# Performance work log

Measured on AMD Instinct MI355X. Metric: run time of the kernel, lower is better.

Reference implementation:

```python
import jax, jax.numpy as jnp
import numpy as np

HIDDEN = 1280
HEADS = 16
HEAD_DIM = HIDDEN // HEADS  # 80
INTER = 4608
DEPTH = 4
WIN = 64                     # tokens per attention window
FULL_BLOCKS = (3,)           # fullatt_block_indexes
EPS = 1e-6
SEQ = 3072


def setup_inputs() -> dict:
    key = jax.random.key(0)
    ks = jax.random.split(key, 20)
    sc = lambda *s: 0.02
    inp = {
        "x": jax.random.normal(ks[0], (SEQ, HIDDEN), jnp.float32),
        "rotary_pos_emb": jax.random.uniform(ks[1], (SEQ, HEAD_DIM // 2), jnp.float32) * 3.0,
        "s_aux": jax.random.normal(ks[2], (HEADS,), jnp.float32),
        "ln1_w": jnp.ones((DEPTH, HIDDEN), jnp.float32),
        "ln1_b": jnp.zeros((DEPTH, HIDDEN), jnp.float32),
        "qkv_w": jax.random.normal(ks[3], (DEPTH, HIDDEN, 3 * HIDDEN), jnp.float32) * 0.02,
        "qkv_b": jnp.zeros((DEPTH, 3 * HIDDEN), jnp.float32),
        "proj_w": jax.random.normal(ks[4], (DEPTH, HIDDEN, HIDDEN), jnp.float32) * 0.02,
        "proj_b": jnp.zeros((DEPTH, HIDDEN), jnp.float32),
        "ln2_w": jnp.ones((DEPTH, HIDDEN), jnp.float32),
        "ln2_b": jnp.zeros((DEPTH, HIDDEN), jnp.float32),
        "gate_w": jax.random.normal(ks[5], (DEPTH, HIDDEN, INTER), jnp.float32) * 0.02,
        "gate_b": jnp.zeros((DEPTH, INTER), jnp.float32),
        "up_w": jax.random.normal(ks[6], (DEPTH, HIDDEN, INTER), jnp.float32) * 0.02,
        "up_b": jnp.zeros((DEPTH, INTER), jnp.float32),
        "down_w": jax.random.normal(ks[7], (DEPTH, INTER, HIDDEN), jnp.float32) * 0.02,
        "down_b": jnp.zeros((DEPTH, HIDDEN), jnp.float32),
    }
    return inp


def _layer_norm(x, w, b):
    mu = jnp.mean(x, axis=-1, keepdims=True)
    var = jnp.mean(jnp.square(x - mu), axis=-1, keepdims=True)
    return (x - mu) * jax.lax.rsqrt(var + EPS) * w + b


def _rotate_half(x):
    x1, x2 = jnp.split(x, 2, axis=-1)
    return jnp.concatenate([-x2, x1], axis=-1)


def _apply_rotary(q, k, rot):
    # q,k: [S, H, D]; rot: [S, D/2]
    emb = jnp.concatenate([rot, rot], axis=-1)          # [S, D]
    cos = jnp.cos(emb)[:, None, :]
    sin = jnp.sin(emb)[:, None, :]
    q = q * cos + _rotate_half(q) * sin
    k = k * cos + _rotate_half(k) * sin
    return q, k


def _attention_with_sinks(q, k, v, s_aux):
    # q,k,v: [B, T, H, D]; block-diagonal within each of B windows.
    scale = 1.0 / jnp.sqrt(jnp.asarray(HEAD_DIM, q.dtype))
    scores = jnp.einsum("bqhd,bkhd->bhqk", q, k) * scale      # [B,H,q,k]
    sink = s_aux[None, :, None]                                # [1,H,1]
    m = jnp.maximum(jnp.max(scores, axis=-1), sink)            # [B,H,q]
    p = jnp.exp(scores - m[..., None])                         # [B,H,q,k]
    denom = jnp.sum(p, axis=-1) + jnp.exp(sink - m)            # [B,H,q]
    out = jnp.einsum("bhqk,bkhd->bqhd", p, v)
    out = out / jnp.transpose(denom, (0, 2, 1))[..., None]     # [B,q,H,D]
    return out


def reference(x, rotary_pos_emb, s_aux, ln1_w, ln1_b, qkv_w, qkv_b, proj_w, proj_b,
              ln2_w, ln2_b, gate_w, gate_b, up_w, up_b, down_w, down_b):
    S = x.shape[0]
    h = x
    for l in range(DEPTH):
        # --- attention ---
        hn = _layer_norm(h, ln1_w[l], ln1_b[l])
        qkv = hn @ qkv_w[l] + qkv_b[l]                          # [S, 3*HIDDEN]
        qkv = qkv.reshape(S, 3, HEADS, HEAD_DIM)
        q, k, v = qkv[:, 0], qkv[:, 1], qkv[:, 2]               # [S,H,D]
        q, k = _apply_rotary(q, k, rotary_pos_emb)
        if l in FULL_BLOCKS:
            B, T = 1, S                                         # full attention
        else:
            B, T = S // WIN, WIN                                # windowed (varlen block-diag)
        qw = q.reshape(B, T, HEADS, HEAD_DIM)
        kw = k.reshape(B, T, HEADS, HEAD_DIM)
        vw = v.reshape(B, T, HEADS, HEAD_DIM)
        o = _attention_with_sinks(qw, kw, vw, s_aux)            # [B,T,H,D]
        o = o.reshape(S, HIDDEN) @ proj_w[l] + proj_b[l]
        h = h + o
        # --- gated SiLU MLP ---
        hn = _layer_norm(h, ln2_w[l], ln2_b[l])
        g = jax.nn.silu(hn @ gate_w[l] + gate_b[l]) * (hn @ up_w[l] + up_b[l])
        h = h + g @ down_w[l] + down_b[l]
    return h
```

## Files before the change

kernel.cpp:

```cpp
#include <hip/hip_runtime.h>
#include <math.h>

typedef unsigned short u16;
typedef unsigned int u32;

using bf16x8 = __attribute__((ext_vector_type(8))) __bf16;
using f32x4  = __attribute__((ext_vector_type(4))) float;

#define SEQ 3072
#define HID 1280
#define NHEADS 16
#define HDIM 80
#define INTER 4608

#define LOG2E 1.44269504088896f
#define M2C   11.5415603f

__device__ __forceinline__ u16 f2bf(float f) {
    __bf16 h = (__bf16)f;
    return __builtin_bit_cast(u16, h);
}

__device__ __forceinline__ void gld16(const void* g, void* l) {
    __builtin_amdgcn_global_load_lds((const __attribute__((address_space(1))) void*)g,
                                     (__attribute__((address_space(3))) void*)l,
                                     16, 0, 0);
}

__device__ __forceinline__ bf16x8 frag8(const u16* base, int row, int ks, int quad) {
    int c = ks * 4 + quad;
    return *(const bf16x8*)&base[(row * 8 + (c ^ (row & 7))) * 8];
}

__global__ __launch_bounds__(256) void transpose_pack(const float* __restrict__ src,
                                                      u16* __restrict__ dst, int K, int N) {
    __shared__ float tile[32][33];
    int l = blockIdx.z;
    const float* s = src + (size_t)l * K * N;
    u16* d = dst + (size_t)l * N * K;
    int n0 = blockIdx.x * 32, k0 = blockIdx.y * 32;
    int tx = threadIdx.x & 31, ty = threadIdx.x >> 5;
#pragma unroll
    for (int i = 0; i < 4; i++) {
        int k = ty + i * 8;
        tile[k][tx] = s[(size_t)(k0 + k) * N + n0 + tx];
    }
    __syncthreads();
#pragma unroll
    for (int i = 0; i < 4; i++) {
        int n = ty + i * 8;
        d[(size_t)(n0 + n) * K + k0 + tx] = f2bf(tile[tx][n]);
    }
}

__global__ __launch_bounds__(256) void transpose_pack_gu(const float* __restrict__ src,
                                                         u16* __restrict__ dst, int K, int N,
                                                         int which) {
    __shared__ float tile[32][33];
    int l = blockIdx.z;
    const float* s = src + (size_t)l * K * N;
    u16* d = dst + (size_t)l * (2 * N) * K;
    int n0 = blockIdx.x * 32, k0 = blockIdx.y * 32;
    int tx = threadIdx.x & 31, ty = threadIdx.x >> 5;
#pragma unroll
    for (int i = 0; i < 4; i++) {
        int k = ty + i * 8;
        tile[k][tx] = s[(size_t)(k0 + k) * N + n0 + tx];
    }
    __syncthreads();
#pragma unroll
    for (int i = 0; i < 4; i++) {
        int n = ty + i * 8;
        int g = n0 + n;
        int n2 = ((g >> 4) << 5) | (g & 15) | (which << 4);
        d[(size_t)n2 * K + k0 + tx] = f2bf(tile[tx][n]);
    }
}

__global__ __launch_bounds__(256) void ln_kernel(const float* __restrict__ x,
                                                 const float* __restrict__ w,
                                                 const float* __restrict__ b,
                                                 u16* __restrict__ out) {
    int row = blockIdx.x;
    const float* xr = x + (size_t)row * HID;
    float v[5]; float s = 0.f, s2 = 0.f;
#pragma unroll
    for (int i = 0; i < 5; i++) { float t = xr[threadIdx.x + i * 256]; v[i] = t; s += t; s2 += t * t; }
#pragma unroll
    for (int off = 32; off > 0; off >>= 1) { s += __shfl_down(s, off); s2 += __shfl_down(s2, off); }
    __shared__ float red[8];
    int wv = threadIdx.x >> 6;
    if ((threadIdx.x & 63) == 0) { red[wv] = s; red[wv + 4] = s2; }
    __syncthreads();
    s  = red[0] + red[1] + red[2] + red[3];
    s2 = red[4] + red[5] + red[6] + red[7];
    float mu  = s * (1.f / HID);
    float var = s2 * (1.f / HID) - mu * mu;
    float rstd = rsqrtf(var + 1e-6f);
#pragma unroll
    for (int i = 0; i < 5; i++) {
        int col = threadIdx.x + i * 256;
        out[(size_t)row * HID + col] = f2bf((v[i] - mu) * rstd * w[col] + b[col]);
    }
}

__global__ __launch_bounds__(256) void qkv_pack(const float* __restrict__ qkv,
                                                const float* __restrict__ rot,
                                                u16* __restrict__ Qp, u16* __restrict__ Kp,
                                                u16* __restrict__ Vt) {
    const float QSC = 0.111803398874989485f * LOG2E;
    int s0 = blockIdx.x * 64, h = blockIdx.y;
    int tid = threadIdx.x;
    __shared__ u16 vlds[80 * 66];
    for (int idx = tid; idx < 64 * 40; idx += 256) {
        int r = idx / 40, d = idx - r * 40;
        const float* base = qkv + (size_t)(s0 + r) * 3840 + h * 80;
        float sn, cs;
        __sincosf(rot[(size_t)(s0 + r) * 40 + d], &sn, &cs);
        float q1 = base[d], q2 = base[d + 40];
        float k1 = base[1280 + d], k2 = base[1280 + d + 40];
        size_t ro = ((size_t)h * SEQ + s0 + r) * 128;
        Qp[ro + d]      = f2bf((q1 * cs - q2 * sn) * QSC);
        Qp[ro + d + 40] = f2bf((q2 * cs + q1 * sn) * QSC);
        Kp[ro + d]      = f2bf(k1 * cs - k2 * sn);
        Kp[ro + d + 40] = f2bf(k2 * cs + k1 * sn);
    }
    for (int idx = tid; idx < 64 * 48; idx += 256) {
        int r = idx / 48, d = 80 + (idx - r * 48);
        size_t ro = ((size_t)h * SEQ + s0 + r) * 128;
        Qp[ro + d] = 0; Kp[ro + d] = 0;
    }
    for (int idx = tid; idx < 64 * 80; idx += 256) {
        int r = idx / 80, d = idx - r * 80;
        vlds[d * 66 + r] = f2bf(qkv[(size_t)(s0 + r) * 3840 + 2560 + h * 80 + d]);
    }
    __syncthreads();
    for (int idx = tid; idx < 80 * 64; idx += 256) {
        int d = idx >> 6, ky = idx & 63;
        Vt[((size_t)h * 80 + d) * SEQ + s0 + ky] = vlds[d * 66 + ky];
    }
}

template<int EPI>
__global__ __launch_bounds__(512, 2) void gemm256(const u16* __restrict__ A,
                                                  const u16* __restrict__ B,
                                                  const float* __restrict__ bias0,
                                                  const float* __restrict__ bias1,
                                                  float* __restrict__ outf,
                                                  u16* __restrict__ outh,
                                                  int N, int K) {
    __shared__ u16 sbuf[73728];
    int tid = threadIdx.x, lane = tid & 63, wave = tid >> 6;
    int quad = lane >> 4, r15 = lane & 15;
    int wm = wave >> 2, wn = wave & 3;

    int nwg = gridDim.x;
    int q8 = nwg >> 3, r8 = nwg & 7;
    int xcd = blockIdx.x & 7, j = blockIdx.x >> 3;
    int wg = (xcd < r8 ? xcd * (q8 + 1) : r8 * (q8 + 1) + (xcd - r8) * q8) + j;
    int bx = wg >> 4, by = wg & 15;
    int mBase = by * 192, nBase = bx * 256;

    int rs = tid >> 3, cs = tid & 7;
    int c0 = cs ^ (rs & 7);
    const u16* gA = A + (size_t)(mBase + rs) * K + c0 * 8;
    const u16* gB = B + (size_t)(nBase + rs) * K + c0 * 8;
    int nK = K >> 6;

    f32x4 acc[6][4] = {};

    auto stageA = [&](int kt, int jl) {
        gld16(gA + (size_t)kt * 64 + (size_t)(jl * 64) * K,
              &sbuf[(kt & 1) * 12288 + jl * 4096 + wave * 512]);
    };
    auto stageB = [&](int kt, int jl) {
        gld16(gB + (size_t)kt * 64 + (size_t)(jl * 64) * K,
              &sbuf[24576 + (kt % 3) * 16384 + jl * 4096 + wave * 512]);
    };

#pragma unroll
    for (int jl = 0; jl < 3; jl++) stageA(0, jl);
#pragma unroll
    for (int jl = 0; jl < 4; jl++) stageB(0, jl);
#pragma unroll
    for (int jl = 0; jl < 4; jl++) stageB(1, jl);
    asm volatile("s_waitcnt vmcnt(4)" ::: "memory");
    __builtin_amdgcn_s_barrier();

    for (int kt = 0; kt < nK; kt++) {
        const u16* Ab = &sbuf[(kt & 1) * 12288];
        const u16* Bb = &sbuf[24576 + (kt % 3) * 16384];
        bool preA = (kt + 1 < nK), preB = (kt + 2 < nK);
#pragma unroll
        for (int ks = 0; ks < 2; ks++) {
            bf16x8 af[6], bf[4];
#pragma unroll
            for (int mi = 0; mi < 6; mi++)
                af[mi] = frag8(Ab, wm * 96 + mi * 16 + r15, ks, quad);
#pragma unroll
            for (int ni = 0; ni < 4; ni++)
                bf[ni] = frag8(Bb, wn * 64 + ni * 16 + r15, ks, quad);
            if (ks == 0) {
                if (preA) { stageA(kt + 1, 0); stageA(kt + 1, 1); stageA(kt + 1, 2); }
            } else {
                if (preB) { stageB(kt + 2, 0); stageB(kt + 2, 1); stageB(kt + 2, 2); stageB(kt + 2, 3); }
            }
            __builtin_amdgcn_s_barrier();
            __builtin_amdgcn_s_setprio(1);
#pragma unroll
            for (int mi = 0; mi < 6; mi++)
#pragma unroll
                for (int ni = 0; ni < 4; ni++)
                    acc[mi][ni] = __builtin_amdgcn_mfma_f32_16x16x32_bf16(
                        af[mi], bf[ni], acc[mi][ni], 0, 0, 0);
            __builtin_amdgcn_s_setprio(0);
            if (ks == 0) __builtin_amdgcn_s_barrier();
        }
        if (preB)      { asm volatile("s_waitcnt vmcnt(4)" ::: "memory"); }
        else if (preA) { asm volatile("s_waitcnt vmcnt(0)" ::: "memory"); }
        __builtin_amdgcn_s_barrier();
    }

    if constexpr (EPI == 0) {
#pragma unroll
        for (int ni = 0; ni < 4; ni++) {
            int col = nBase + wn * 64 + ni * 16 + r15;
            float bv = bias0[col];
#pragma unroll
            for (int a = 0; a < 6; a++)
#pragma unroll
                for (int jj = 0; jj < 4; jj++) {
                    int row = mBase + wm * 96 + a * 16 + quad * 4 + jj;
                    outf[(size_t)row * N + col] = acc[a][ni][jj] + bv;
                }
        }
    } else {
#pragma unroll
        for (int pp = 0; pp < 2; pp++) {
            int col = (nBase >> 1) + wn * 32 + pp * 16 + r15;
            float gb = bias0[col], ub = bias1[col];
#pragma unroll
            for (int a = 0; a < 6; a++)
#pragma unroll
                for (int jj = 0; jj < 4; jj++) {
                    int row = mBase + wm * 96 + a * 16 + quad * 4 + jj;
                    float g = acc[a][2 * pp][jj] + gb;
                    float u = acc[a][2 * pp + 1][jj] + ub;
                    float sg = g / (1.f + __expf(-g));
                    outh[(size_t)row * INTER + col] = f2bf(sg * u);
                }
        }
    }
}

template<int BM, int EPI>
__global__ __launch_bounds__(512, 2) void gemm8(const u16* __restrict__ A,
                                                const u16* __restrict__ B,
                                                const float* __restrict__ bias0,
                                                const float* __restrict__ bias1,
                                                const float* __restrict__ res,
                                                float* __restrict__ outf,
                                                u16* __restrict__ outh,
                                                int N, int K) {
    constexpr int MT   = 3072 / BM;
    constexpr int MF   = BM / 32;
    constexpr int LA   = BM / 64;
    constexpr int LT   = LA + 2;
    constexpr int ABUF = BM * 64;
    constexpr int BUFU = ABUF + 8192;
    __shared__ u16 sbuf[3 * BUFU];

    int tid = threadIdx.x, lane = tid & 63, wave = tid >> 6;
    int quad = lane >> 4, r15 = lane & 15;
    int wm = wave >> 2, wn = wave & 3;

    int nwg = gridDim.x;
    int q8 = nwg >> 3, r8 = nwg & 7;
    int xcd = blockIdx.x & 7, j = blockIdx.x >> 3;
    int wg = (xcd < r8 ? xcd * (q8 + 1) : r8 * (q8 + 1) + (xcd - r8) * q8) + j;
    int bx = wg / MT, by = wg % MT;
    int mBase = by * BM, nBase = bx * 128;

    int rs = tid >> 3, cs = tid & 7;
    int c0 = cs ^ (rs & 7);
    const u16* gA = A + (size_t)(mBase + rs) * K + c0 * 8;
    const u16* gB = B + (size_t)(nBase + rs) * K + c0 * 8;
    int nK = K >> 6;

    f32x4 acc[MF][2] = {};

    auto stage1 = [&](int kt, int jl) {
        int b = kt % 3;
        if (jl < LA) {
            gld16(gA + (size_t)kt * 64 + (size_t)(jl * 64) * K,
                  &sbuf[b * BUFU + jl * 4096 + wave * 512]);
        } else {
            int i = jl - LA;
            gld16(gB + (size_t)kt * 64 + (size_t)(i * 64) * K,
                  &sbuf[b * BUFU + ABUF + i * 4096 + wave * 512]);
        }
    };

#pragma unroll
    for (int jl = 0; jl < LT; jl++) stage1(0, jl);
#pragma unroll
    for (int jl = 0; jl < LT; jl++) stage1(1, jl);
    asm volatile("s_waitcnt vmcnt(4)" ::: "memory");
    __builtin_amdgcn_s_barrier();

    for (int kt = 0; kt < nK; kt++) {
        const u16* Ab = &sbuf[(kt % 3) * BUFU];
        const u16* Bb = Ab + ABUF;
        bool pre = (kt + 2 < nK);
#pragma unroll
        for (int ks = 0; ks < 2; ks++) {
            bf16x8 af[MF], bf[2];
#pragma unroll
            for (int mi = 0; mi < MF; mi++)
                af[mi] = frag8(Ab, wm * (BM / 2) + mi * 16 + r15, ks, quad);
#pragma unroll
            for (int ni = 0; ni < 2; ni++)
                bf[ni] = frag8(Bb, wn * 32 + ni * 16 + r15, ks, quad);
            if (pre) {
#pragma unroll
                for (int jl = 0; jl < LT / 2; jl++) stage1(kt + 2, ks * (LT / 2) + jl);
            }
            __builtin_amdgcn_s_barrier();
            __builtin_amdgcn_s_setprio(1);
#pragma unroll
            for (int mi = 0; mi < MF; mi++)
#pragma unroll
                for (int ni = 0; ni < 2; ni++)
                    acc[mi][ni] = __builtin_amdgcn_mfma_f32_16x16x32_bf16(
                        af[mi], bf[ni], acc[mi][ni], 0, 0, 0);
            __builtin_amdgcn_s_setprio(0);
            if (ks == 0) __builtin_amdgcn_s_barrier();
        }
        if (pre) {
            asm volatile("s_waitcnt vmcnt(4)" ::: "memory");
        } else if (kt + 1 < nK) {
            asm volatile("s_waitcnt vmcnt(0)" ::: "memory");
        }
        __builtin_amdgcn_s_barrier();
    }

#pragma unroll
    for (int ni = 0; ni < 2; ni++) {
        int col = nBase + wn * 32 + ni * 16 + r15;
        float bv = bias0[col];
#pragma unroll
        for (int mi = 0; mi < MF; mi++)
#pragma unroll
            for (int jj = 0; jj < 4; jj++) {
                int row = mBase + wm * (BM / 2) + mi * 16 + quad * 4 + jj;
                float v = acc[mi][ni][jj] + bv;
                if constexpr (EPI == 1) v += res[(size_t)row * N + col];
                outf[(size_t)row * N + col] = v;
            }
    }
}

template<int QR>
__global__ __launch_bounds__(256) void attn_kernel(const u16* __restrict__ Qp,
                                                   const u16* __restrict__ Kp,
                                                   const u16* __restrict__ Vt,
                                                   const float* __restrict__ s_aux,
                                                   u16* __restrict__ out) {
    constexpr int MH = QR / 64;
    __shared__ u16 q_lds[QR * 128];
    __shared__ u16 k_lds[8192];
    __shared__ u16 v_lds[5120];
    __shared__ u16 p_lds[QR * 72];

    int qt = blockIdx.x, h = blockIdx.y;
    int tid = threadIdx.x, lane = tid & 63, wave = tid >> 6;
    int quad = lane >> 4, r15 = lane & 15;

    const u16* Qh = Qp + (size_t)h * SEQ * 128;
    const u16* Kh = Kp + (size_t)h * SEQ * 128;
    const u16* Vh = Vt + (size_t)h * 80 * SEQ;

    {
        int q0 = qt * QR;
#pragma unroll
        for (int i = 0; i < QR / 16; i++) {
            int slot = i * 256 + tid;
            int row = slot >> 4, cc = slot & 15;
            int c = cc ^ (row & 7);
            gld16(Qh + (size_t)(q0 + row) * 128 + c * 8, &q_lds[(i * 256 + wave * 64) * 8]);
        }
    }
    __syncthreads();
    bf16x8 aq[MH][3];
#pragma unroll
    for (int mh = 0; mh < MH; mh++)
#pragma unroll
        for (int ks = 0; ks < 3; ks++) {
            int row = wave * (16 * MH) + mh * 16 + r15;
            int c = ks * 4 + quad;
            aq[mh][ks] = *(const bf16x8*)&q_lds[(row * 16 + (c ^ (row & 7))) * 8];
        }

    float l_j[MH][4] = {};
    f32x4 ov[MH][5] = {};

    int nT = (QR == 64) ? 1 : (SEQ / 64);
    int tBase = (QR == 64) ? qt : 0;
    for (int t = 0; t < nT; t++) {
        int key0 = (tBase + t) * 64;
        __syncthreads();
#pragma unroll
        for (int i = 0; i < 4; i++) {
            int slot = i * 256 + wave * 64 + lane;
            int row = slot >> 4, cc = slot & 15;
            int c = cc ^ (row & 7);
            gld16(Kh + (size_t)(key0 + row) * 128 + c * 8, &k_lds[(i * 256 + wave * 64) * 8]);
        }
#pragma unroll
        for (int i = 0; i < 2; i++) {
            int slot = i * 256 + wave * 64 + lane;
            int row = slot >> 3, cc = slot & 7;
            int c = cc ^ (row & 7);
            gld16(Vh + (size_t)row * SEQ + key0 + c * 8, &v_lds[(i * 256 + wave * 64) * 8]);
        }
        if (wave < 2) {
            int slot = 512 + wave * 64 + lane;
            int row = slot >> 3, cc = slot & 7;
            int c = cc ^ (row & 7);
            gld16(Vh + (size_t)row * SEQ + key0 + c * 8, &v_lds[(512 + wave * 64) * 8]);
        }
        __syncthreads();

        f32x4 sc[MH][4] = {};
#pragma unroll
        for (int nt = 0; nt < 4; nt++)
#pragma unroll
            for (int ks = 0; ks < 3; ks++) {
                int row = nt * 16 + r15;
                int c = ks * 4 + quad;
                bf16x8 bk = *(const bf16x8*)&k_lds[(row * 16 + (c ^ (row & 7))) * 8];
#pragma unroll
                for (int mh = 0; mh < MH; mh++)
                    sc[mh][nt] = __builtin_amdgcn_mfma_f32_16x16x32_bf16(aq[mh][ks], bk, sc[mh][nt], 0, 0, 0);
            }
#pragma unroll
        for (int mh = 0; mh < MH; mh++)
#pragma unroll
            for (int nt = 0; nt < 4; nt++)
#pragma unroll
                for (int jj = 0; jj < 4; jj++) {
                    float p = __builtin_amdgcn_exp2f(sc[mh][nt][jj] - M2C);
                    l_j[mh][jj] += p;
                    p_lds[(wave * 16 * MH + mh * 16 + quad * 4 + jj) * 72 + nt * 16 + r15] = f2bf(p);
                }
        asm volatile("s_waitcnt lgkmcnt(0)" ::: "memory");
        bf16x8 ap[MH][2];
#pragma unroll
        for (int mh = 0; mh < MH; mh++)
#pragma unroll
            for (int ks = 0; ks < 2; ks++)
                ap[mh][ks] = *(const bf16x8*)&p_lds[(wave * 16 * MH + mh * 16 + r15) * 72 + ks * 32 + quad * 8];
#pragma unroll
        for (int t5 = 0; t5 < 5; t5++)
#pragma unroll
            for (int ks = 0; ks < 2; ks++) {
                int d = t5 * 16 + r15;
                int c = ks * 4 + quad;
                bf16x8 bv = *(const bf16x8*)&v_lds[(d * 8 + (c ^ (d & 7))) * 8];
#pragma unroll
                for (int mh = 0; mh < MH; mh++)
                    ov[mh][t5] = __builtin_amdgcn_mfma_f32_16x16x32_bf16(ap[mh][ks], bv, ov[mh][t5], 0, 0, 0);
            }
    }
#pragma unroll
    for (int mh = 0; mh < MH; mh++)
#pragma unroll
        for (int off = 1; off < 16; off <<= 1)
#pragma unroll
            for (int jj = 0; jj < 4; jj++)
                l_j[mh][jj] += __shfl_xor(l_j[mh][jj], off, 64);
    float sink = s_aux[h];
    float se = __builtin_amdgcn_exp2f(sink * LOG2E - M2C);
#pragma unroll
    for (int mh = 0; mh < MH; mh++)
#pragma unroll
        for (int jj = 0; jj < 4; jj++) l_j[mh][jj] = 1.f / (l_j[mh][jj] + se);
#pragma unroll
    for (int mh = 0; mh < MH; mh++)
#pragma unroll
        for (int t5 = 0; t5 < 5; t5++)
#pragma unroll
            for (int jj = 0; jj < 4; jj++) {
                int row = qt * QR + wave * 16 * MH + mh * 16 + quad * 4 + jj;
                int d = t5 * 16 + r15;
                out[(size_t)row * HID + h * 80 + d] = f2bf(ov[mh][t5][jj] * l_j[mh][jj]);
            }
}

__global__ __launch_bounds__(256) void copy4_kernel(const float4* __restrict__ src,
                                                    float4* __restrict__ dst) {
    size_t i = (size_t)blockIdx.x * 256 + threadIdx.x;
    dst[i] = src[i];
}

extern "C" void kernel_launch(void* const* d_in, const int* in_sizes, int n_in,
                              void* d_out, int out_size, void* d_ws, size_t ws_size,
                              hipStream_t stream) {
    const float* x      = (const float*)d_in[0];
    const float* rot    = (const float*)d_in[1];
    const float* s_aux  = (const float*)d_in[2];
    const float* ln1_w  = (const float*)d_in[3];
    const float* ln1_b  = (const float*)d_in[4];
    const float* qkv_w  = (const float*)d_in[5];
    const float* qkv_b  = (const float*)d_in[6];
    const float* proj_w = (const float*)d_in[7];
    const float* proj_b = (const float*)d_in[8];
    const float* ln2_w  = (const float*)d_in[9];
    const float* ln2_b  = (const float*)d_in[10];
    const float* gate_w = (const float*)d_in[11];
    const float* gate_b = (const float*)d_in[12];
    const float* up_w   = (const float*)d_in[13];
    const float* up_b   = (const float*)d_in[14];
    const float* down_w = (const float*)d_in[15];
    const float* down_b = (const float*)d_in[16];

    char* ws = (char*)d_ws;
    size_t off = 0;
    auto alloc = [&](size_t n) -> char* {
        char* p = ws + off; off += (n + 255) & ~(size_t)255; return p;
    };
    u16* wt_qkv  = (u16*)alloc((size_t)4 * 3840 * 1280 * 2);
    u16* wt_proj = (u16*)alloc((size_t)4 * 1280 * 1280 * 2);
    u16* wt_gu   = (u16*)alloc((size_t)4 * 9216 * 1280 * 2);
    u16* wt_down = (u16*)alloc((size_t)4 * 1280 * 4608 * 2);
    float* h     = (float*)alloc((size_t)3072 * 1280 * 4);
    u16*  xn     = (u16*)alloc((size_t)3072 * 1280 * 2);
    float* gbuf  = (float*)alloc((size_t)3072 * 4608 * 4);
    float* qkvb  = gbuf;
    u16*  attnb  = (u16*)alloc((size_t)3072 * 1280 * 2);
    float* ubuf  = (float*)alloc((size_t)3072 * 4608 * 4);
    u16*  mbuf   = (u16*)alloc((size_t)3072 * 4608 * 2);
    u16* Qp  = (u16*)ubuf;
    u16* Kp  = Qp + (size_t)NHEADS * SEQ * 128;
    u16* Vtp = Kp + (size_t)NHEADS * SEQ * 128;

    transpose_pack<<<dim3(120, 40, 4), 256, 0, stream>>>(qkv_w,  wt_qkv,  1280, 3840);
    transpose_pack<<<dim3(40,  40, 4), 256, 0, stream>>>(proj_w, wt_proj, 1280, 1280);
    transpose_pack_gu<<<dim3(144, 40, 4), 256, 0, stream>>>(gate_w, wt_gu, 1280, 4608, 0);
    transpose_pack_gu<<<dim3(144, 40, 4), 256, 0, stream>>>(up_w,   wt_gu, 1280, 4608, 1);
    transpose_pack<<<dim3(40, 144, 4), 256, 0, stream>>>(down_w, wt_down, 4608, 1280);

    copy4_kernel<<<3840, 256, 0, stream>>>((const float4*)x, (float4*)h);

    for (int l = 0; l < 4; l++) {
        ln_kernel<<<3072, 256, 0, stream>>>(h, ln1_w + l * 1280, ln1_b + l * 1280, xn);
        gemm256<0><<<240, 512, 0, stream>>>(xn, wt_qkv + (size_t)l * 3840 * 1280,
                                            qkv_b + l * 3840, nullptr,
                                            qkvb, nullptr, 3840, 1280);
        qkv_pack<<<dim3(48, 16), 256, 0, stream>>>(qkvb, rot, Qp, Kp, Vtp);
        if (l == 3)
            attn_kernel<128><<<dim3(SEQ / 128, 16), 256, 0, stream>>>(Qp, Kp, Vtp, s_aux, attnb);
        else
            attn_kernel<64><<<dim3(SEQ / 64, 16), 256, 0, stream>>>(Qp, Kp, Vtp, s_aux, attnb);
        gemm8<128, 1><<<240, 512, 0, stream>>>(attnb, wt_proj + (size_t)l * 1280 * 1280,
                                               proj_b + l * 1280, nullptr, h,
                                               h, nullptr, 1280, 1280);
        ln_kernel<<<3072, 256, 0, stream>>>(h, ln2_w + l * 1280, ln2_b + l * 1280, xn);
        gemm256<2><<<576, 512, 0, stream>>>(xn, wt_gu + (size_t)l * 9216 * 1280,
                                            gate_b + l * 4608, up_b + l * 4608,
                                            nullptr, mbuf, 9216, 1280);
        float* outp = (l == 3) ? (float*)d_out : h;
        gemm8<128, 1><<<240, 512, 0, stream>>>(mbuf, wt_down + (size_t)l * 4608 * 1280,
                                               down_b + l * 1280, nullptr, h,
                                               outp, nullptr, 1280, 4608);
    }
}
```

Before: 1.467 ms.

## Restructure GEMM pipelines with split A/B buffering and prefetch attention K/V tiles

The 256-wide GEMM drops the mid-iteration barriers, precomputes swizzled LDS offsets, and splits its k-step loop into two explicit halves. The proj/down GEMM is specialised to 128x128 tiles with double-buffered A and triple-buffered B, a smaller shared allocation, and launch bounds raised to 4 blocks per CU. The attention kernel now prefetches the next K/V tile into registers while computing on the current one, then writes it to LDS between barriers. Together these aim to hide memory latency and cut barrier stalls, at the cost of more register pressure and a risk of LDS races once the intermediate barriers are gone.

Measured after the change: 1.522 ms. +3.8%, slower.

```diff
diff --git a/kernel.cpp b/kernel.cpp
--- a/kernel.cpp
+++ b/kernel.cpp
@@ -167,6 +167,21 @@
     const u16* gB = B + (size_t)(nBase + rs) * K + c0 * 8;
     int nK = K >> 6;
 
+    int offA[2][6], offB[2][4];
+#pragma unroll
+    for (int ks = 0; ks < 2; ks++) {
+#pragma unroll
+        for (int mi = 0; mi < 6; mi++) {
+            int row = wm * 96 + mi * 16 + r15, c = ks * 4 + quad;
+            offA[ks][mi] = (row * 8 + (c ^ (row & 7))) * 8;
+        }
+#pragma unroll
+        for (int ni = 0; ni < 4; ni++) {
+            int row = wn * 64 + ni * 16 + r15, c = ks * 4 + quad;
+            offB[ks][ni] = (row * 8 + (c ^ (row & 7))) * 8;
+        }
+    }
+
     f32x4 acc[6][4] = {};
 
     auto stageA = [&](int kt, int jl) {
@@ -182,6 +197,7 @@
     for (int jl = 0; jl < 3; jl++) stageA(0, jl);
 #pragma unroll
     for (int jl = 0; jl < 4; jl++) stageB(0, jl);
+    asm volatile("" ::: "memory");
 #pragma unroll
     for (int jl = 0; jl < 4; jl++) stageB(1, jl);
     asm volatile("s_waitcnt vmcnt(4)" ::: "memory");
@@ -191,21 +207,14 @@
         const u16* Ab = &sbuf[(kt & 1) * 12288];
         const u16* Bb = &sbuf[24576 + (kt % 3) * 16384];
         bool preA = (kt + 1 < nK), preB = (kt + 2 < nK);
-#pragma unroll
-        for (int ks = 0; ks < 2; ks++) {
+        {
             bf16x8 af[6], bf[4];
 #pragma unroll
-            for (int mi = 0; mi < 6; mi++)
-                af[mi] = frag8(Ab, wm * 96 + mi * 16 + r15, ks, quad);
-#pragma unroll
-            for (int ni = 0; ni < 4; ni++)
-                bf[ni] = frag8(Bb, wn * 64 + ni * 16 + r15, ks, quad);
-            if (ks == 0) {
-                if (preA) { stageA(kt + 1, 0); stageA(kt + 1, 1); stageA(kt + 1, 2); }
-            } else {
-                if (preB) { stageB(kt + 2, 0); stageB(kt + 2, 1); stageB(kt + 2, 2); stageB(kt + 2, 3); }
-            }
-            __builtin_amdgcn_s_barrier();
+            for (int mi = 0; mi < 6; mi++) af[mi] = *(const bf16x8*)&Ab[offA[0][mi]];
+#pragma unroll
+            for (int ni = 0; ni < 4; ni++) bf[ni] = *(const bf16x8*)&Bb[offB[0][ni]];
+            if (preA) { stageA(kt + 1, 0); stageA(kt + 1, 1); stageA(kt + 1, 2); }
+            asm volatile("" ::: "memory");
             __builtin_amdgcn_s_setprio(1);
 #pragma unroll
             for (int mi = 0; mi < 6; mi++)
@@ -214,7 +223,22 @@
                     acc[mi][ni] = __builtin_amdgcn_mfma_f32_16x16x32_bf16(
                         af[mi], bf[ni], acc[mi][ni], 0, 0, 0);
             __builtin_amdgcn_s_setprio(0);
-            if (ks == 0) __builtin_amdgcn_s_barrier();
+        }
+        {
+            bf16x8 af[6], bf[4];
+#pragma unroll
+            for (int mi = 0; mi < 6; mi++) af[mi] = *(const bf16x8*)&Ab[offA[1][mi]];
+#pragma unroll
+            for (int ni = 0; ni < 4; ni++) bf[ni] = *(const bf16x8*)&Bb[offB[1][ni]];
+            if (preB) { stageB(kt + 2, 0); stageB(kt + 2, 1); stageB(kt + 2, 2); stageB(kt + 2, 3); }
+            __builtin_amdgcn_s_setprio(1);
+#pragma unroll
+            for (int mi = 0; mi < 6; mi++)
+#pragma unroll
+                for (int ni = 0; ni < 4; ni++)
+                    acc[mi][ni] = __builtin_amdgcn_mfma_f32_16x16x32_bf16(
+                        af[mi], bf[ni], acc[mi][ni], 0, 0, 0);
+            __builtin_amdgcn_s_setprio(0);
         }
         if (preB)      { asm volatile("s_waitcnt vmcnt(4)" ::: "memory"); }
         else if (preA) { asm volatile("s_waitcnt vmcnt(0)" ::: "memory"); }
@@ -253,23 +277,14 @@
     }
 }
 
-template<int BM, int EPI>
-__global__ __launch_bounds__(512, 2) void gemm8(const u16* __restrict__ A,
+template<int EPI>
+__global__ __launch_bounds__(512, 4) void gemm8(const u16* __restrict__ A,
                                                 const u16* __restrict__ B,
                                                 const float* __restrict__ bias0,
-                                                const float* __restrict__ bias1,
                                                 const float* __restrict__ res,
                                                 float* __restrict__ outf,
-                                                u16* __restrict__ outh,
                                                 int N, int K) {
-    constexpr int MT   = 3072 / BM;
-    constexpr int MF   = BM / 32;
-    constexpr int LA   = BM / 64;
-    constexpr int LT   = LA + 2;
-    constexpr int ABUF = BM * 64;
-    constexpr int BUFU = ABUF + 8192;
-    __shared__ u16 sbuf[3 * BUFU];
-
+    __shared__ u16 sbuf[40960];
     int tid = threadIdx.x, lane = tid & 63, wave = tid >> 6;
     int quad = lane >> 4, r15 = lane & 15;
     int wm = wave >> 2, wn = wave & 3;
@@ -278,8 +293,8 @@
     int q8 = nwg >> 3, r8 = nwg & 7;
     int xcd = blockIdx.x & 7, j = blockIdx.x >> 3;
     int wg = (xcd < r8 ? xcd * (q8 + 1) : r8 * (q8 + 1) + (xcd - r8) * q8) + j;
-    int bx = wg / MT, by = wg % MT;
-    int mBase = by * BM, nBase = bx * 128;
+    int bx = wg / 24, by = wg % 24;
+    int mBase = by * 128, nBase = bx * 128;
 
     int rs = tid >> 3, cs = tid & 7;
     int c0 = cs ^ (rs & 7);
@@ -287,60 +302,81 @@
     const u16* gB = B + (size_t)(nBase + rs) * K + c0 * 8;
     int nK = K >> 6;
 
-    f32x4 acc[MF][2] = {};
-
-    auto stage1 = [&](int kt, int jl) {
-        int b = kt % 3;
-        if (jl < LA) {
-            gld16(gA + (size_t)kt * 64 + (size_t)(jl * 64) * K,
-                  &sbuf[b * BUFU + jl * 4096 + wave * 512]);
-        } else {
-            int i = jl - LA;
-            gld16(gB + (size_t)kt * 64 + (size_t)(i * 64) * K,
-                  &sbuf[b * BUFU + ABUF + i * 4096 + wave * 512]);
-        }
+    int offA[2][4], offB[2][2];
+#pragma unroll
+    for (int ks = 0; ks < 2; ks++) {
+#pragma unroll
+        for (int mi = 0; mi < 4; mi++) {
+            int row = wm * 64 + mi * 16 + r15, c = ks * 4 + quad;
+            offA[ks][mi] = (row * 8 + (c ^ (row & 7))) * 8;
+        }
+#pragma unroll
+        for (int ni = 0; ni < 2; ni++) {
+            int row = wn * 32 + ni * 16 + r15, c = ks * 4 + quad;
+            offB[ks][ni] = (row * 8 + (c ^ (row & 7))) * 8;
+        }
+    }
+
+    f32x4 acc[4][2] = {};
+
+    auto stageA = [&](int kt, int jl) {
+        gld16(gA + (size_t)kt * 64 + (size_t)(jl * 64) * K,
+              &sbuf[(kt & 1) * 8192 + jl * 4096 + wave * 512]);
     };
-
-#pragma unroll
-    for (int jl = 0; jl < LT; jl++) stage1(0, jl);
-#pragma unroll
-    for (int jl = 0; jl < LT; jl++) stage1(1, jl);
-    asm volatile("s_waitcnt vmcnt(4)" ::: "memory");
+    auto stageB = [&](int kt, int jl) {
+        gld16(gB + (size_t)kt * 64 + (size_t)(jl * 64) * K,
+              &sbuf[16384 + (kt % 3) * 8192 + jl * 4096 + wave * 512]);
+    };
+
+#pragma unroll
+    for (int jl = 0; jl < 2; jl++) stageA(0, jl);
+#pragma unroll
+    for (int jl = 0; jl < 2; jl++) stageB(0, jl);
+    asm volatile("" ::: "memory");
+#pragma unroll
+    for (int jl = 0; jl < 2; jl++) stageB(1, jl);
+    asm volatile("s_waitcnt vmcnt(2)" ::: "memory");
     __builtin_amdgcn_s_barrier();
 
     for (int kt = 0; kt < nK; kt++) {
-        const u16* Ab = &sbuf[(kt % 3) * BUFU];
-        const u16* Bb = Ab + ABUF;
-        bool pre = (kt + 2 < nK);
-#pragma unroll
-        for (int ks = 0; ks < 2; ks++) {
-            bf16x8 af[MF], bf[2];
-#pragma unroll
-            for (int mi = 0; mi < MF; mi++)
-                af[mi] = frag8(Ab, wm * (BM / 2) + mi * 16 + r15, ks, quad);
-#pragma unroll
-            for (int ni = 0; ni < 2; ni++)
-                bf[ni] = frag8(Bb, wn * 32 + ni * 16 + r15, ks, quad);
-            if (pre) {
-#pragma unroll
-                for (int jl = 0; jl < LT / 2; jl++) stage1(kt + 2, ks * (LT / 2) + jl);
-            }
-            __builtin_amdgcn_s_barrier();
+        const u16* Ab = &sbuf[(kt & 1) * 8192];
+        const u16* Bb = &sbuf[16384 + (kt % 3) * 8192];
+        bool preA = (kt + 1 < nK), preB = (kt + 2 < nK);
+        {
+            bf16x8 af[4], bf[2];
+#pragma unroll
+            for (int mi = 0; mi < 4; mi++) af[mi] = *(const bf16x8*)&Ab[offA[0][mi]];
+#pragma unroll
+            for (int ni = 0; ni < 2; ni++) bf[ni] = *(const bf16x8*)&Bb[offB[0][ni]];
+            if (preA) { stageA(kt + 1, 0); stageA(kt + 1, 1); }
+            asm volatile("" ::: "memory");
             __builtin_amdgcn_s_setprio(1);
 #pragma unroll
-            for (int mi = 0; mi < MF; mi++)
+            for (int mi = 0; mi < 4; mi++)
 #pragma unroll
                 for (int ni = 0; ni < 2; ni++)
                     acc[mi][ni] = __builtin_amdgcn_mfma_f32_16x16x32_bf16(
                         af[mi], bf[ni], acc[mi][ni], 0, 0, 0);
             __builtin_amdgcn_s_setprio(0);
-            if (ks == 0) __builtin_amdgcn_s_barrier();
-        }
-        if (pre) {
-            asm volatile("s_waitcnt vmcnt(4)" ::: "memory");
-        } else if (kt + 1 < nK) {
-            asm volatile("s_waitcnt vmcnt(0)" ::: "memory");
-        }
+        }
+        {
+            bf16x8 af[4], bf[2];
+#pragma unroll
+            for (int mi = 0; mi < 4; mi++) af[mi] = *(const bf16x8*)&Ab[offA[1][mi]];
+#pragma unroll
+            for (int ni = 0; ni < 2; ni++) bf[ni] = *(const bf16x8*)&Bb[offB[1][ni]];
+            if (preB) { stageB(kt + 2, 0); stageB(kt + 2, 1); }
+            __builtin_amdgcn_s_setprio(1);
+#pragma unroll
+            for (int mi = 0; mi < 4; mi++)
+#pragma unroll
+                for (int ni = 0; ni < 2; ni++)
+                    acc[mi][ni] = __builtin_amdgcn_mfma_f32_16x16x32_bf16(
+                        af[mi], bf[ni], acc[mi][ni], 0, 0, 0);
+            __builtin_amdgcn_s_setprio(0);
+        }
+        if (preB)      { asm volatile("s_waitcnt vmcnt(2)" ::: "memory"); }
+        else if (preA) { asm volatile("s_waitcnt vmcnt(0)" ::: "memory"); }
         __builtin_amdgcn_s_barrier();
     }
 
@@ -349,10 +385,10 @@
         int col = nBase + wn * 32 + ni * 16 + r15;
         float bv = bias0[col];
 #pragma unroll
-        for (int mi = 0; mi < MF; mi++)
+        for (int mi = 0; mi < 4; mi++)
 #pragma unroll
             for (int jj = 0; jj < 4; jj++) {
-                int row = mBase + wm * (BM / 2) + mi * 16 + quad * 4 + jj;
+                int row = mBase + wm * 64 + mi * 16 + quad * 4 + jj;
                 float v = acc[mi][ni][jj] + bv;
                 if constexpr (EPI == 1) v += res[(size_t)row * N + col];
                 outf[(size_t)row * N + col] = v;
@@ -406,30 +442,52 @@
 
     int nT = (QR == 64) ? 1 : (SEQ / 64);
     int tBase = (QR == 64) ? qt : 0;
+
+    {
+        int key0 = tBase * 64;
+#pragma unroll
+        for (int i = 0; i < 4; i++) {
+            int slot = i * 256 + tid;
+            int row = slot >> 4, c = (slot & 15) ^ (row & 7);
+            gld16(Kh + (size_t)(key0 + row) * 128 + c * 8, &k_lds[(i * 256 + wave * 64) * 8]);
+        }
+#pragma unroll
+        for (int i = 0; i < 2; i++) {
+            int slot = i * 256 + tid;
+            int row = slot >> 3, c = (slot & 7) ^ (row & 7);
+            gld16(Vh + (size_t)row * SEQ + key0 + c * 8, &v_lds[(i * 256 + wave * 64) * 8]);
+        }
+        if (tid < 128) {
+            int slot = 512 + tid;
+            int row = slot >> 3, c = (slot & 7) ^ (row & 7);
+            gld16(Vh + (size_t)row * SEQ + key0 + c * 8, &v_lds[(512 + (tid >> 6) * 64) * 8]);
+        }
+    }
+    __syncthreads();
+
     for (int t = 0; t < nT; t++) {
-        int key0 = (tBase + t) * 64;
-        __syncthreads();
-#pragma unroll
-        for (int i = 0; i < 4; i++) {
-            int slot = i * 256 + wave * 64 + lane;
-            int row = slot >> 4, cc = slot & 15;
-            int c = cc ^ (row & 7);
-            gld16(Kh + (size_t)(key0 + row) * 128 + c * 8, &k_lds[(i * 256 + wave * 64) * 8]);
-        }
-#pragma unroll
-        for (int i = 0; i < 2; i++) {
-            int slot = i * 256 + wave * 64 + lane;
-            int row = slot >> 3, cc = slot & 7;
-            int c = cc ^ (row & 7);
-            gld16(Vh + (size_t)row * SEQ + key0 + c * 8, &v_lds[(i * 256 + wave * 64) * 8]);
-        }
-        if (wave < 2) {
-            int slot = 512 + wave * 64 + lane;
-            int row = slot >> 3, cc = slot & 7;
-            int c = cc ^ (row & 7);
-            gld16(Vh + (size_t)row * SEQ + key0 + c * 8, &v_lds[(512 + wave * 64) * 8]);
-        }
-        __syncthreads();
+        bool pf = (t + 1 < nT);
+        uint4 kreg[4], vreg[3];
+        if (pf) {
+            int keyN = (tBase + t + 1) * 64;
+#pragma unroll
+            for (int i = 0; i < 4; i++) {
+                int slot = i * 256 + tid;
+                int row = slot >> 4, c = (slot & 15) ^ (row & 7);
+                kreg[i] = *(const uint4*)(Kh + (size_t)(keyN + row) * 128 + c * 8);
+            }
+#pragma unroll
+            for (int i = 0; i < 2; i++) {
+                int slot = i * 256 + tid;
+                int row = slot >> 3, c = (slot & 7) ^ (row & 7);
+                vreg[i] = *(const uint4*)(Vh + (size_t)row * SEQ + keyN + c * 8);
+            }
+            if (tid < 128) {
+                int slot = 512 + tid;
+                int row = slot >> 3, c = (slot & 7) ^ (row & 7);
+                vreg[2] = *(const uint4*)(Vh + (size_t)row * SEQ + keyN + c * 8);
+            }
+        }
 
         f32x4 sc[MH][4] = {};
 #pragma unroll
@@ -471,6 +529,16 @@
                 for (int mh = 0; mh < MH; mh++)
                     ov[mh][t5] = __builtin_amdgcn_mfma_f32_16x16x32_bf16(ap[mh][ks], bv, ov[mh][t5], 0, 0, 0);
             }
+
+        if (pf) {
+            __syncthreads();
+#pragma unroll
+            for (int i = 0; i < 4; i++) ((uint4*)k_lds)[i * 256 + tid] = kreg[i];
+#pragma unroll
+            for (int i = 0; i < 2; i++) ((uint4*)v_lds)[i * 256 + tid] = vreg[i];
+            if (tid < 128) ((uint4*)v_lds)[512 + tid] = vreg[2];
+            __syncthreads();
+        }
     }
 #pragma unroll
     for (int mh = 0; mh < MH; mh++)
@@ -562,16 +630,14 @@
             attn_kernel<128><<<dim3(SEQ / 128, 16), 256, 0, stream>>>(Qp, Kp, Vtp, s_aux, attnb);
         else
             attn_kernel<64><<<dim3(SEQ / 64, 16), 256, 0, stream>>>(Qp, Kp, Vtp, s_aux, attnb);
-        gemm8<128, 1><<<240, 512, 0, stream>>>(attnb, wt_proj + (size_t)l * 1280 * 1280,
-                                               proj_b + l * 1280, nullptr, h,
-                                               h, nullptr, 1280, 1280);
+        gemm8<1><<<240, 512, 0, stream>>>(attnb, wt_proj + (size_t)l * 1280 * 1280,
+                                          proj_b + l * 1280, h, h, 1280, 1280);
         ln_kernel<<<3072, 256, 0, stream>>>(h, ln2_w + l * 1280, ln2_b + l * 1280, xn);
         gemm256<2><<<576, 512, 0, stream>>>(xn, wt_gu + (size_t)l * 9216 * 1280,
                                             gate_b + l * 4608, up_b + l * 4608,
                                             nullptr, mbuf, 9216, 1280);
         float* outp = (l == 3) ? (float*)d_out : h;
-        gemm8<128, 1><<<240, 512, 0, stream>>>(mbuf, wt_down + (size_t)l * 4608 * 1280,
-                                               down_b + l * 1280, nullptr, h,
-                                               outp, nullptr, 1280, 4608);
-    }
-}
+        gemm8<1><<<240, 512, 0, stream>>>(mbuf, wt_down + (size_t)l * 4608 * 1280,
+                                          down_b + l * 1280, h, outp, 1280, 4608);
+    }
+}
```
